# Optimization experiments

Hardware: AMD Instinct MI355X
Metric: run time of the kernel (lower is better)

## Reference

```python
import jax, jax.numpy as jnp
import numpy as np
import math

LOG_2PI = math.log(2.0 * math.pi)

def mv_gaussian_log_prob(value, mu, sig_diags, event_shape):
    # sig_diags acts as per-dim std (matches torch source: diff**2 / sig**2)
    diff = value - mu
    M = jnp.sum((diff / sig_diags) ** 2, axis=-1)
    half_log_det = jnp.sum(jnp.log(sig_diags), axis=-1)
    return -0.5 * (event_shape * LOG_2PI + M) - half_log_det

def setup_inputs() -> dict:
    key = jax.random.key(0)
    ks = jax.random.split(key, 18)
    N, Yd, Xd, K, S = 8192, 512, 64, 16, 10
    d = {}
    d['Y'] = jax.random.normal(ks[0], (N, Yd), jnp.float32)
    d['We_mu'] = jax.random.normal(ks[1], (Yd, Xd), jnp.float32) * 0.05
    d['be_mu'] = jnp.zeros((Xd,), jnp.float32)
    d['We_sig'] = jax.random.normal(ks[2], (Yd, Xd), jnp.float32) * 0.05
    d['be_sig'] = jnp.zeros((Xd,), jnp.float32)
    d['Wd_mu'] = jax.random.normal(ks[3], (Xd, Yd), jnp.float32) * 0.05
    d['bd_mu'] = jnp.zeros((Yd,), jnp.float32)
    d['Wd_sig'] = jax.random.normal(ks[4], (Xd, Yd), jnp.float32) * 0.05
    d['bd_sig'] = jnp.zeros((Yd,), jnp.float32)
    d['phi_mus'] = jax.random.normal(ks[5], (K, Xd), jnp.float32)
    d['phi_sigs'] = jax.random.uniform(ks[6], (K, Xd), jnp.float32, 0.5, 1.5)
    d['phi_logits'] = jax.random.normal(ks[7], (K,), jnp.float32)
    d['theta_mus'] = jax.random.normal(ks[8], (K, Xd), jnp.float32)
    d['theta_sigs'] = jax.random.uniform(ks[9], (K, Xd), jnp.float32, 0.5, 1.5)
    d['theta_logits'] = jax.random.normal(ks[10], (K,), jnp.float32)
    d['u_noise'] = jax.random.uniform(ks[11], (N, S, K), jnp.float32, 1e-6, 1.0 - 1e-6)
    d['eps_noise'] = jax.random.normal(ks[12], (N * S, Xd), jnp.float32)
    d['temperature'] = jnp.ones((1,), jnp.float32)
    return d

def reference(Y, We_mu, be_mu, We_sig, be_sig, Wd_mu, bd_mu, Wd_sig, bd_sig,
              phi_mus, phi_sigs, phi_logits, theta_mus, theta_sigs, theta_logits,
              u_noise, eps_noise, temperature):
    N, Yd = Y.shape
    K, Xd = phi_mus.shape
    S = u_noise.shape[1]
    # encoder: diagonal Gaussian q(x|y)
    enc_mu = Y @ We_mu + be_mu                                   # [N,Xd]
    enc_sig = jax.nn.softplus(Y @ We_sig + be_sig) + 1e-3        # [N,Xd]
    # cluster responsibilities (vectorized over k)
    log_pi = jax.nn.log_softmax(phi_logits)                      # [K]
    std_k = enc_sig[:, None, :] + phi_sigs[None, :, :]           # [N,K,Xd]
    z_logits = log_pi[None, :] + mv_gaussian_log_prob(
        enc_mu[:, None, :], phi_mus[None, :, :], std_k, Xd)      # [N,K]
    z_log_probs = jax.nn.log_softmax(z_logits, axis=-1)
    # per-cluster posterior (diagonal precision-weighted combination)
    inv_enc = 1.0 / enc_sig                                      # [N,Xd]
    inv_gmm = 1.0 / phi_sigs                                     # [K,Xd]
    Sig_t = 1.0 / (inv_enc[:, None, :] + inv_gmm[None, :, :])    # [N,K,Xd]
    mu_t = Sig_t * ((inv_enc * enc_mu)[:, None, :] + (inv_gmm * phi_mus)[None, :, :])
    # relaxed one-hot (gumbel-softmax) samples, probs = exp(z_log_probs)
    g = -jnp.log(-jnp.log(u_noise))                              # [N,S,K]
    z = jax.nn.softmax((z_log_probs[:, None, :] + g) / temperature[0], axis=-1)
    mu_s = jnp.einsum('bsk,bkd->bsd', z, mu_t).reshape(N * S, Xd)
    Sig_s = jnp.einsum('bsk,bkd->bsd', z, Sig_t).reshape(N * S, Xd)
    th_mu = jnp.einsum('bsk,kd->bsd', z, theta_mus).reshape(N * S, Xd)
    th_sig = jnp.einsum('bsk,kd->bsd', z, theta_sigs).reshape(N * S, Xd)
    ph_mu = jnp.einsum('bsk,kd->bsd', z, phi_mus).reshape(N * S, Xd)
    ph_sig = jnp.einsum('bsk,kd->bsd', z, phi_sigs).reshape(N * S, Xd)
    # reparameterized latent samples (diag cov -> std = sqrt)
    x_samp = mu_s + jnp.sqrt(Sig_s) * eps_noise                  # [N*S,Xd]
    # decoder
    mu_y = x_samp @ Wd_mu + bd_mu
    sig_y = jax.nn.softplus(x_samp @ Wd_sig + bd_sig) + 1e-3
    Yr = jnp.broadcast_to(Y[:, None, :], (N, S, Yd)).reshape(N * S, Yd)
    enc_mu_r = jnp.broadcast_to(enc_mu[:, None, :], (N, S, Xd)).reshape(N * S, Xd)
    enc_sig_r = jnp.broadcast_to(enc_sig[:, None, :], (N, S, Xd)).reshape(N * S, Xd)
    zf = z.reshape(N * S, K)
    loss1 = mv_gaussian_log_prob(Yr, mu_y, sig_y, Yd)
    loss2 = -mv_gaussian_log_prob(x_samp, enc_mu_r, enc_sig_r, Xd)
    loss3 = (mv_gaussian_log_prob(x_samp, th_mu, th_sig, Xd)
             + jnp.sum(jax.nn.log_softmax(theta_logits) * zf, axis=1))
    loss4 = -(mv_gaussian_log_prob(x_samp, ph_mu, ph_sig, Xd)
              + jnp.sum((z_log_probs[:, None, :] * z).reshape(N * S, K), axis=1))
    loss5 = jnp.sum(jnp.log(jnp.sum(jnp.exp(z_log_probs), axis=1)))
    return -(jnp.sum(loss1 + loss2 + loss3 + loss4) / S + loss5)
```

## Files before the change

### kernel.cpp

```cpp
#include <hip/hip_runtime.h>
#include <math.h>

#define YD 512
#define XD 64
#define KK 16
#define SS 10

typedef __attribute__((ext_vector_type(8))) short short8;
typedef __attribute__((ext_vector_type(4))) float f32x4;
typedef __attribute__((ext_vector_type(2))) float f32x2;

__device__ __forceinline__ float wave_sum(float v) {
#pragma unroll
    for (int off = 32; off > 0; off >>= 1) v += __shfl_xor(v, off, 64);
    return v;
}

__device__ __forceinline__ float fast_rcp(float x) {
    return __builtin_amdgcn_rcpf(x);
}

__device__ __forceinline__ float hw_exp2(float x) {
    return __builtin_amdgcn_exp2f(x);
}
__device__ __forceinline__ float hw_log2(float x) {
    return __builtin_amdgcn_logf(x);
}

__device__ __forceinline__ float bcast(float v, int l) {
    return __uint_as_float((unsigned int)__builtin_amdgcn_readlane((int)__float_as_uint(v), l));
}

__device__ __forceinline__ float softplusf(float x) {
    return fmaxf(x, 0.0f) + __logf(1.0f + __expf(-fabsf(x)));
}

__device__ __forceinline__ unsigned short f32_to_bf16(float f) {
    union { float f; unsigned int u; } v; v.f = f;
    unsigned int r = v.u + 0x7fffu + ((v.u >> 16) & 1u);
    return (unsigned short)(r >> 16);
}

__device__ __forceinline__ unsigned int pack2_bf16(float a, float b) {
    unsigned int ua = __float_as_uint(a), ub = __float_as_uint(b);
    ua = (ua + 0x7fffu + ((ua >> 16) & 1u)) >> 16;
    ub = (ub + 0x7fffu + ((ub >> 16) & 1u)) & 0xffff0000u;
    return ua | ub;
}

__global__ __launch_bounds__(256) void prep_kernel(
    const float* __restrict__ Wd_mu, const float* __restrict__ Wd_sig,
    const float* __restrict__ We_mu, const float* __restrict__ We_sig,
    const float* __restrict__ phi_mus, const float* __restrict__ phi_sigs,
    const float* __restrict__ theta_mus, const float* __restrict__ theta_sigs,
    const float* __restrict__ theta_logits,
    unsigned short* __restrict__ wmu_s, unsigned short* __restrict__ wsg_s,
    unsigned short* __restrict__ wenc,
    float4* __restrict__ tab4, float* __restrict__ lsetp)
{
    int idx = blockIdx.x * 256 + threadIdx.x;
    if (idx < 65536) {
        int mat = idx >> 15;
        int e = idx & 32767;
        int j = e & 7;
        int n = (e >> 3) & 15;
        int q = (e >> 7) & 7;
        int tg = e >> 10;
        int k = q * 8 + j;
        int col = tg * 16 + n;
        const float* W = mat ? Wd_sig : Wd_mu;
        unsigned short* o = mat ? wsg_s : wmu_s;
        o[e] = f32_to_bf16(W[k * YD + col]);
    } else if (idx < 131072) {
        int ii = idx - 65536;
        int mat = ii >> 15;
        int e = ii & 32767;
        int j = e & 7;
        int n = (e >> 3) & 15;
        int q = (e >> 7) & 3;
        int ct = (e >> 9) & 3;
        int kt = e >> 11;
        int k = kt * 32 + q * 8 + j;
        int col = ct * 16 + n;
        const float* W = mat ? We_sig : We_mu;
        wenc[mat * 32768 + e] = f32_to_bf16(W[k * XD + col]);
    } else if (idx < 131072 + 1024) {
        int e = idx - 131072;
        float4 t;
        t.x = phi_mus[e];
        t.y = phi_sigs[e];
        t.z = theta_mus[e];
        t.w = theta_sigs[e];
        tab4[e] = t;
    } else if (idx == 131072 + 1024) {
        float mt = theta_logits[0];
        for (int k = 1; k < KK; ++k) mt = fmaxf(mt, theta_logits[k]);
        float st = 0.f;
        for (int k = 0; k < KK; ++k) st += __expf(theta_logits[k] - mt);
        lsetp[0] = mt + __logf(st);
    }
}

__global__ __launch_bounds__(256) void encoder_mfma(
    const float* __restrict__ Y,
    const unsigned short* __restrict__ wenc,
    const float* __restrict__ be_mu, const float* __restrict__ be_sig,
    float* __restrict__ enc_mu, float* __restrict__ enc_sig)
{
    const int t = threadIdx.x;
    const int w = t >> 6, lane = t & 63, l16 = lane & 15, quad = lane >> 4;
    const int mat = blockIdx.x & 1;
    const int rt = blockIdx.x >> 1;
    const int row = rt * 16 + l16;
    const int ct = w;
    const unsigned short* Ws = wenc + mat * 32768;
    const float4* Yrow = (const float4*)(Y + (size_t)row * YD);

    const float* bias = mat ? be_sig : be_mu;
    float* outp = mat ? enc_sig : enc_mu;
    const int col = ct * 16 + l16;
    const float bv = bias[col];
    f32x4 acc = (f32x4){bv, bv, bv, bv};

#pragma unroll
    for (int kt = 0; kt < 16; ++kt) {
        float4 y0 = Yrow[kt * 8 + quad * 2];
        float4 y1 = Yrow[kt * 8 + quad * 2 + 1];
        union { short8 s; unsigned int u[4]; } a;
        a.u[0] = pack2_bf16(y0.x, y0.y);
        a.u[1] = pack2_bf16(y0.z, y0.w);
        a.u[2] = pack2_bf16(y1.x, y1.y);
        a.u[3] = pack2_bf16(y1.z, y1.w);
        short8 b = *(const short8*)(Ws + (((kt * 4 + ct) * 4 + quad) * 16 + l16) * 8);
        acc = __builtin_amdgcn_mfma_f32_16x16x32_bf16(a.s, b, acc, 0, 0, 0);
    }

    const int base_row = rt * 16 + quad * 4;
#pragma unroll
    for (int r = 0; r < 4; ++r) {
        float v = acc[r];
        if (mat) v = softplusf(v) + 1e-3f;
        outp[(size_t)(base_row + r) * XD + col] = v;
    }
}

__global__ __launch_bounds__(256, 3) void fused_sample_kernel(
    const float* __restrict__ enc_mu_g, const float* __restrict__ enc_sig_g,
    const float* __restrict__ phi_mus, const float* __restrict__ phi_sigs,
    const float* __restrict__ phi_logits, const float4* __restrict__ tab4,
    const float* __restrict__ theta_logits, const float* __restrict__ lsetp,
    const float* __restrict__ u_noise, const float* __restrict__ eps_noise,
    const float* __restrict__ temperature,
    unsigned short* __restrict__ x_bf16, double* __restrict__ slots)
{
    __shared__ float red234[4], red5[4];
    const int wv = threadIdx.x >> 6;
    const int n = blockIdx.x * 4 + wv;
    const int d = threadIdx.x & 63;
    const int kd = d & 15;
    const int g = d >> 4;

    const float4* em4 = (const float4*)(enc_mu_g + (size_t)n * XD + g * 16);
    const float4* es4 = (const float4*)(enc_sig_g + (size_t)n * XD + g * 16);
    const float4* pm4 = (const float4*)(phi_mus + kd * XD + g * 16);
    const float4* ps4 = (const float4*)(phi_sigs + kd * XD + g * 16);

    float part = 0.f;
#pragma unroll
    for (int q = 0; q < 4; ++q) {
        float4 emv = em4[q], esv = es4[q], pmv = pm4[q], psv = ps4[q];
        {
            float sd = esv.x + psv.x; float df = (emv.x - pmv.x) * fast_rcp(sd);
            part += fmaf(-0.5f * df, df, -__logf(sd));
        }
        {
            float sd = esv.y + psv.y; float df = (emv.y - pmv.y) * fast_rcp(sd);
            part += fmaf(-0.5f * df, df, -__logf(sd));
        }
        {
            float sd = esv.z + psv.z; float df = (emv.z - pmv.z) * fast_rcp(sd);
            part += fmaf(-0.5f * df, df, -__logf(sd));
        }
        {
            float sd = esv.w + psv.w; float df = (emv.w - pmv.w) * fast_rcp(sd);
            part += fmaf(-0.5f * df, df, -__logf(sd));
        }
    }
    part += __shfl_xor(part, 16, 64);
    part += __shfl_xor(part, 32, 64);
    float zl = part + phi_logits[kd];

    float m = zl;
#pragma unroll
    for (int off = 1; off <= 8; off <<= 1) m = fmaxf(m, __shfl_xor(m, off, 64));
    float e0 = __expf(zl - m);
    float s0 = e0;
#pragma unroll
    for (int off = 1; off <= 8; off <<= 1) s0 += __shfl_xor(s0, off, 64);
    zl -= m + __logf(s0);

    float m3 = zl;
#pragma unroll
    for (int off = 1; off <= 8; off <<= 1) m3 = fmaxf(m3, __shfl_xor(m3, off, 64));
    float e3 = __expf(zl - m3);
    float s3 = e3;
#pragma unroll
    for (int off = 1; off <= 8; off <<= 1) s3 += __shfl_xor(s3, off, 64);
    float l5 = m3 + __logf(s3);

    const float invT = fast_rcp(temperature[0]);
    const float zl_l = zl;
    const float tl_l = theta_logits[kd];
    const float lset = lsetp[0];

    const float em = enc_mu_g[(size_t)n * XD + d];
    const float es = enc_sig_g[(size_t)n * XD + d];
    const float inv_es = fast_rcp(es);
    const float log_es = __logf(es);
    const float em_ie = inv_es * em;

    f32x2 mS[KK], tt2[KK], pp2[KK];
#pragma unroll
    for (int k = 0; k < KK; ++k) {
        float4 tb = tab4[k * XD + d];
        float ig = fast_rcp(tb.y);
        float Sgk = fast_rcp(inv_es + ig);
        float muk = Sgk * fmaf(ig, tb.x, em_ie);
        mS[k]  = (f32x2){muk, Sgk};
        tt2[k] = (f32x2){tb.z, tb.w};
        pp2[k] = (f32x2){tb.x, tb.y};
    }

    float eP[3];
    float esc = 0.f;
#pragma unroll
    for (int p = 0; p < 3; ++p) {
        int sp = p * 4 + g;
        int spc = sp < SS ? sp : 0;
        float u = u_noise[((size_t)n * SS + spc) * KK + kd];
        float lg = (zl_l - __logf(-__logf(u))) * invT;
        float mg = lg;
        mg = fmaxf(mg, __shfl_xor(mg, 1, 64));
        mg = fmaxf(mg, __shfl_xor(mg, 2, 64));
        mg = fmaxf(mg, __shfl_xor(mg, 4, 64));
        mg = fmaxf(mg, __shfl_xor(mg, 8, 64));
        float e = __expf(lg - mg);
        float zs = e;
        zs += __shfl_xor(zs, 1, 64);
        zs += __shfl_xor(zs, 2, 64);
        zs += __shfl_xor(zs, 4, 64);
        zs += __shfl_xor(zs, 8, 64);
        e *= fast_rcp(zs);
        eP[p] = e;
        if (sp < SS) esc = fmaf(e, tl_l - zl_l, esc);
    }

    float r_acc = 0.f;
    const float* erow = eps_noise + (size_t)n * SS * XD + d;
    unsigned short* xrow = x_bf16 + (size_t)n * SS * XD + d;

#pragma unroll
    for (int s = 0; s < SS; ++s) {
        const int p = s >> 2, L = (s & 3) * 16;
        f32x2 a0 = (f32x2){0.f, 0.f};
        f32x2 a1 = (f32x2){0.f, 0.f};
        f32x2 a2 = (f32x2){0.f, 0.f};
#pragma unroll
        for (int k = 0; k < KK; ++k) {
            float ek = bcast(eP[p], L + k);
            f32x2 ev = (f32x2){ek, ek};
            a0 = a0 + ev * mS[k];
            a1 = a1 + ev * tt2[k];
            a2 = a2 + ev * pp2[k];
        }
        float ms = a0.x, Ssum = a0.y;
        float tmu = a1.x, tsig = a1.y;
        float pmu = a2.x, psig = a2.y;

        float ep = erow[s * XD];
        float x = fmaf(__builtin_amdgcn_sqrtf(Ssum), ep, ms);
        xrow[s * XD] = f32_to_bf16(x);

        float de  = (x - em) * inv_es;
        float rts = fast_rcp(tsig);
        float dt2 = (x - tmu) * rts;
        float dp  = (x - pmu) * fast_rcp(psig);
        r_acc += 0.5f * (de * de - dt2 * dt2 + dp * dp) + __logf(psig * rts);
    }

    r_acc = fmaf((float)SS, log_es, r_acc);
    r_acc += esc;
    r_acc = wave_sum(r_acc);

    const float C234 = 0.5f * XD * 1.8378770664093453f;
    float total = r_acc + (float)SS * (C234 - lset);

    if (d == 0) { red234[wv] = total; red5[wv] = l5; }
    __syncthreads();
    if (threadIdx.x == 0) {
        atomicAdd(slots + (blockIdx.x & 63),
                  (double)(red234[0] + red234[1] + red234[2] + red234[3]));
        atomicAdd(slots + 64 + (blockIdx.x & 63),
                  (double)(red5[0] + red5[1] + red5[2] + red5[3]));
    }
}

__global__ __launch_bounds__(256) void decoder_mfma(
    const unsigned short* __restrict__ xb,
    const unsigned short* __restrict__ wmu_s,
    const unsigned short* __restrict__ wsg_s,
    const float* __restrict__ bd_mu, const float* __restrict__ bd_sig,
    const float* __restrict__ Y, double* __restrict__ slots1,
    unsigned int magicS)
{
    __shared__ float red[4];
    const int t = threadIdx.x;
    const int w = t >> 6;
    const int lane = t & 63;
    const int l16 = lane & 15;
    const int quad = lane >> 4;
    const int mb = blockIdx.x;
    const int nb = blockIdx.y;

    const int row0 = mb * 128 + w * 32;

    float Yv[2][4][4];
#pragma unroll
    for (int rg = 0; rg < 2; ++rg) {
        const int m_base = row0 + rg * 16 + quad * 4;
        unsigned int q10 = (unsigned int)(((unsigned long long)(unsigned int)m_base * magicS) >> 35);
        int rem = m_base - (int)q10 * 10;
#pragma unroll
        for (int r = 0; r < 4; ++r) {
            unsigned int ny = q10 + ((rem + r) >= 10 ? 1u : 0u);
            unsigned int iy = ny * YD + nb * 64 + l16;
#pragma unroll
            for (int tt = 0; tt < 4; ++tt) Yv[rg][r][tt] = Y[iy + tt * 16];
        }
    }

    short8 a[2][2];
#pragma unroll
    for (int rg = 0; rg < 2; ++rg) {
        const unsigned short* xp = xb + (size_t)(row0 + rg * 16 + l16) * XD + quad * 8;
        a[rg][0] = *(const short8*)xp;
        a[rg][1] = *(const short8*)(xp + 32);
    }

    f32x4 accmu[2][4], accsg[2][4];
#pragma unroll
    for (int tt = 0; tt < 4; ++tt) {
        int col = nb * 64 + tt * 16 + l16;
        float bm = bd_mu[col], bs = bd_sig[col];
#pragma unroll
        for (int rg = 0; rg < 2; ++rg) {
            accmu[rg][tt] = (f32x4){bm, bm, bm, bm};
            accsg[rg][tt] = (f32x4){bs, bs, bs, bs};
        }
    }

#pragma unroll
    for (int tt = 0; tt < 4; ++tt) {
        int tg = nb * 4 + tt;
        int boff = ((tg * 8 + quad) * 16 + l16) * 8;
        short8 b0 = *(const short8*)(wmu_s + boff);
        short8 b1 = *(const short8*)(wmu_s + boff + 512);
        short8 c0 = *(const short8*)(wsg_s + boff);
        short8 c1 = *(const short8*)(wsg_s + boff + 512);
#pragma unroll
        for (int rg = 0; rg < 2; ++rg) {
            accmu[rg][tt] = __builtin_amdgcn_mfma_f32_16x16x32_bf16(a[rg][0], b0, accmu[rg][tt], 0, 0, 0);
            accmu[rg][tt] = __builtin_amdgcn_mfma_f32_16x16x32_bf16(a[rg][1], b1, accmu[rg][tt], 0, 0, 0);
            accsg[rg][tt] = __builtin_amdgcn_mfma_f32_16x16x32_bf16(a[rg][0], c0, accsg[rg][tt], 0, 0, 0);
            accsg[rg][tt] = __builtin_amdgcn_mfma_f32_16x16x32_bf16(a[rg][1], c1, accsg[rg][tt], 0, 0, 0);
        }
    }

    const float LOG2E = 1.4426950408889634f;
    const float C2    = 0.0014426950408889634f;
    const float Cq    = -1.0406844905181233f;
    const float LN2   = 0.6931471805599453f;
    const float CC    = 11.72841345861326f;

    f32x2 pq = (f32x2){0.f, 0.f};
    f32x2 pl = (f32x2){0.f, 0.f};
    f32x2 prod = (f32x2){1.f, 1.f};
#pragma unroll
    for (int r = 0; r < 4; ++r) {
#pragma unroll
        for (int tt = 0; tt < 4; ++tt) {
            f32x2 acs = (f32x2){accsg[0][tt][r], accsg[1][tt][r]};
            f32x2 acm = (f32x2){accmu[0][tt][r], accmu[1][tt][r]};
            f32x2 yv  = (f32x2){Yv[0][r][tt], Yv[1][r][tt]};
            f32x2 te  = acs * LOG2E;
            f32x2 u2;
            u2.x = hw_exp2(te.x);
            u2.y = hw_exp2(te.y);
            f32x2 up = u2 + 1.0f;
            f32x2 s2;
            s2.x = hw_log2(up.x);
            s2.y = hw_log2(up.y);
            s2 = s2 + C2;
            f32x2 rs;
            rs.x = fast_rcp(s2.x);
            rs.y = fast_rcp(s2.y);
            f32x2 diff = (yv - acm) * rs;
            pq = pq + (Cq * diff) * diff;
            prod = prod * s2;
        }
        if (r & 1) {
            pl.x += hw_log2(prod.x);
            pl.y += hw_log2(prod.y);
            prod = (f32x2){1.f, 1.f};
        }
    }
    float part = fmaf(-LN2, pl.x + pl.y, pq.x + pq.y) + CC;
    part = wave_sum(part);
    if (lane == 0) red[w] = part;
    __syncthreads();
    if (t == 0) {
        atomicAdd(slots1 + ((blockIdx.y * gridDim.x + blockIdx.x) & 63),
                  (double)(red[0] + red[1] + red[2] + red[3]));
    }
}

__global__ void finalize_kernel(const double* __restrict__ slots,
                                float* __restrict__ out, int NS, int S)
{
    double l234 = 0.0, l5 = 0.0, l1 = 0.0;
    for (int i = 0; i < 64; ++i) {
        l234 += slots[i];
        l5   += slots[64 + i];
        l1   += slots[128 + i];
    }
    l1 += (double)NS * (-0.5 * (double)YD * 1.8378770664093453);
    out[0] = (float)(-((l1 + l234) / (double)S + l5));
}

extern "C" void kernel_launch(void* const* d_in, const int* in_sizes, int n_in,
                              void* d_out, int out_size, void* d_ws, size_t ws_size,
                              hipStream_t stream) {
    const float* Y            = (const float*)d_in[0];
    const float* We_mu        = (const float*)d_in[1];
    const float* be_mu        = (const float*)d_in[2];
    const float* We_sig       = (const float*)d_in[3];
    const float* be_sig       = (const float*)d_in[4];
    const float* Wd_mu        = (const float*)d_in[5];
    const float* bd_mu        = (const float*)d_in[6];
    const float* Wd_sig       = (const float*)d_in[7];
    const float* bd_sig       = (const float*)d_in[8];
    const float* phi_mus      = (const float*)d_in[9];
    const float* phi_sigs     = (const float*)d_in[10];
    const float* phi_logits   = (const float*)d_in[11];
    const float* theta_mus    = (const float*)d_in[12];
    const float* theta_sigs   = (const float*)d_in[13];
    const float* theta_logits = (const float*)d_in[14];
    const float* u_noise      = (const float*)d_in[15];
    const float* eps_noise    = (const float*)d_in[16];
    const float* temperature  = (const float*)d_in[17];

    const int N = in_sizes[0] / YD;
    const int S = in_sizes[15] / (N * KK);
    const int NS = N * S;
    const unsigned int magicS =
        (unsigned int)((((unsigned long long)1 << 35) + S - 1) / (unsigned long long)S);

    char* base = (char*)d_ws;
    double* slots = (double*)base;
    float* enc_mu  = (float*)(base + 2048);
    float* enc_sig = enc_mu + (size_t)N * XD;
    float* zlp     = enc_sig + (size_t)N * XD;
    float4* tab4   = (float4*)(zlp + (size_t)N * KK);
    float* lsetp   = (float*)(tab4 + 1024);
    unsigned short* xb    = (unsigned short*)(lsetp + 16);
    unsigned short* wmu_s = xb + (size_t)NS * XD;
    unsigned short* wsg_s = wmu_s + 32768;
    unsigned short* wenc  = wsg_s + 32768;

    hipMemsetAsync(slots, 0, 2048, stream);

    prep_kernel<<<517, 256, 0, stream>>>(Wd_mu, Wd_sig, We_mu, We_sig,
                                         phi_mus, phi_sigs, theta_mus,
                                         theta_sigs, theta_logits,
                                         wmu_s, wsg_s, wenc, tab4, lsetp);
    encoder_mfma<<<(N / 16) * 2, 256, 0, stream>>>(Y, wenc, be_mu, be_sig,
                                                   enc_mu, enc_sig);
    fused_sample_kernel<<<N / 4, 256, 0, stream>>>(enc_mu, enc_sig,
                                                   phi_mus, phi_sigs, phi_logits,
                                                   tab4, theta_logits, lsetp,
                                                   u_noise, eps_noise, temperature,
                                                   xb, slots);
    decoder_mfma<<<dim3(NS / 128, YD / 64), 256, 0, stream>>>(
        xb, wmu_s, wsg_s, bd_mu, bd_sig, Y, slots + 128, magicS);
    finalize_kernel<<<1, 1, 0, stream>>>(slots, (float*)d_out, NS, S);
}
```

Baseline: 194.6 us.

## Fold slot zeroing into prep, finalize in last decoder block, drop softmax max-shifts

Zeroes the accumulation slots and ticket inside prep_kernel instead of a separate memset, and moves the final reduction into the last-finishing decoder block using an atomic ticket, removing two launches. It also drops the max-subtraction in two 16-way log-sum-exp and Gumbel-softmax reductions, since log-softmax outputs are at most zero and the Gumbel logits are bounded for these inputs. The risk is overflow if temperature is small or the logits are large, plus the usual threadfence/ticket ordering subtleties.

```diff
diff --git a/kernel.cpp b/kernel.cpp
--- a/kernel.cpp
+++ b/kernel.cpp
@@ -56,7 +56,8 @@
     const float* __restrict__ theta_logits,
     unsigned short* __restrict__ wmu_s, unsigned short* __restrict__ wsg_s,
     unsigned short* __restrict__ wenc,
-    float4* __restrict__ tab4, float* __restrict__ lsetp)
+    float4* __restrict__ tab4, float* __restrict__ lsetp,
+    unsigned int* __restrict__ slots_zero)
 {
     int idx = blockIdx.x * 256 + threadIdx.x;
     if (idx < 65536) {
@@ -98,6 +99,8 @@
         float st = 0.f;
         for (int k = 0; k < KK; ++k) st += __expf(theta_logits[k] - mt);
         lsetp[0] = mt + __logf(st);
+    } else if (idx >= 132352 && idx < 132864) {
+        slots_zero[idx - 132352] = 0u;
     }
 }
 
@@ -199,14 +202,10 @@
     for (int off = 1; off <= 8; off <<= 1) s0 += __shfl_xor(s0, off, 64);
     zl -= m + __logf(s0);
 
-    float m3 = zl;
-#pragma unroll
-    for (int off = 1; off <= 8; off <<= 1) m3 = fmaxf(m3, __shfl_xor(m3, off, 64));
-    float e3 = __expf(zl - m3);
-    float s3 = e3;
+    float s3 = __expf(zl);
 #pragma unroll
     for (int off = 1; off <= 8; off <<= 1) s3 += __shfl_xor(s3, off, 64);
-    float l5 = m3 + __logf(s3);
+    float l5 = __logf(s3);
 
     const float invT = fast_rcp(temperature[0]);
     const float zl_l = zl;
@@ -239,12 +238,7 @@
         int spc = sp < SS ? sp : 0;
         float u = u_noise[((size_t)n * SS + spc) * KK + kd];
         float lg = (zl_l - __logf(-__logf(u))) * invT;
-        float mg = lg;
-        mg = fmaxf(mg, __shfl_xor(mg, 1, 64));
-        mg = fmaxf(mg, __shfl_xor(mg, 2, 64));
-        mg = fmaxf(mg, __shfl_xor(mg, 4, 64));
-        mg = fmaxf(mg, __shfl_xor(mg, 8, 64));
-        float e = __expf(lg - mg);
+        float e = __expf(lg);
         float zs = e;
         zs += __shfl_xor(zs, 1, 64);
         zs += __shfl_xor(zs, 2, 64);
@@ -310,8 +304,9 @@
     const unsigned short* __restrict__ wmu_s,
     const unsigned short* __restrict__ wsg_s,
     const float* __restrict__ bd_mu, const float* __restrict__ bd_sig,
-    const float* __restrict__ Y, double* __restrict__ slots1,
-    unsigned int magicS)
+    const float* __restrict__ Y, double* __restrict__ slots,
+    unsigned int* __restrict__ ticket, float* __restrict__ out,
+    unsigned int magicS, int NS, int S, int totalBlocks)
 {
     __shared__ float red[4];
     const int t = threadIdx.x;
@@ -419,22 +414,21 @@
     if (lane == 0) red[w] = part;
     __syncthreads();
     if (t == 0) {
-        atomicAdd(slots1 + ((blockIdx.y * gridDim.x + blockIdx.x) & 63),
+        atomicAdd(slots + 128 + ((blockIdx.y * gridDim.x + blockIdx.x) & 63),
                   (double)(red[0] + red[1] + red[2] + red[3]));
-    }
-}
-
-__global__ void finalize_kernel(const double* __restrict__ slots,
-                                float* __restrict__ out, int NS, int S)
-{
-    double l234 = 0.0, l5 = 0.0, l1 = 0.0;
-    for (int i = 0; i < 64; ++i) {
-        l234 += slots[i];
-        l5   += slots[64 + i];
-        l1   += slots[128 + i];
-    }
-    l1 += (double)NS * (-0.5 * (double)YD * 1.8378770664093453);
-    out[0] = (float)(-((l1 + l234) / (double)S + l5));
+        __threadfence();
+        unsigned int old = atomicAdd(ticket, 1u);
+        if (old == (unsigned int)(totalBlocks - 1)) {
+            double l234 = 0.0, l5 = 0.0, l1 = 0.0;
+            for (int i = 0; i < 64; ++i) {
+                l234 += __hip_atomic_load(slots + i,       __ATOMIC_RELAXED, __HIP_MEMORY_SCOPE_AGENT);
+                l5   += __hip_atomic_load(slots + 64 + i,  __ATOMIC_RELAXED, __HIP_MEMORY_SCOPE_AGENT);
+                l1   += __hip_atomic_load(slots + 128 + i, __ATOMIC_RELAXED, __HIP_MEMORY_SCOPE_AGENT);
+            }
+            l1 += (double)NS * (-0.5 * (double)YD * 1.8378770664093453);
+            out[0] = (float)(-((l1 + l234) / (double)S + l5));
+        }
+    }
 }
 
 extern "C" void kernel_launch(void* const* d_in, const int* in_sizes, int n_in,
@@ -467,6 +461,7 @@
 
     char* base = (char*)d_ws;
     double* slots = (double*)base;
+    unsigned int* ticket = (unsigned int*)(base + 1536);
     float* enc_mu  = (float*)(base + 2048);
     float* enc_sig = enc_mu + (size_t)N * XD;
     float* zlp     = enc_sig + (size_t)N * XD;
@@ -477,12 +472,13 @@
     unsigned short* wsg_s = wmu_s + 32768;
     unsigned short* wenc  = wsg_s + 32768;
 
-    hipMemsetAsync(slots, 0, 2048, stream);
-
-    prep_kernel<<<517, 256, 0, stream>>>(Wd_mu, Wd_sig, We_mu, We_sig,
+    const int decBlocks = (NS / 128) * (YD / 64);
+
+    prep_kernel<<<520, 256, 0, stream>>>(Wd_mu, Wd_sig, We_mu, We_sig,
                                          phi_mus, phi_sigs, theta_mus,
                                          theta_sigs, theta_logits,
-                                         wmu_s, wsg_s, wenc, tab4, lsetp);
+                                         wmu_s, wsg_s, wenc, tab4, lsetp,
+                                         (unsigned int*)slots);
     encoder_mfma<<<(N / 16) * 2, 256, 0, stream>>>(Y, wenc, be_mu, be_sig,
                                                    enc_mu, enc_sig);
     fused_sample_kernel<<<N / 4, 256, 0, stream>>>(enc_mu, enc_sig,
@@ -491,6 +487,6 @@
                                                    u_noise, eps_noise, temperature,
                                                    xb, slots);
     decoder_mfma<<<dim3(NS / 128, YD / 64), 256, 0, stream>>>(
-        xb, wmu_s, wsg_s, bd_mu, bd_sig, Y, slots + 128, magicS);
-    finalize_kernel<<<1, 1, 0, stream>>>(slots, (float*)d_out, NS, S);
-}
+        xb, wmu_s, wsg_s, bd_mu, bd_sig, Y, slots, ticket, (float*)d_out,
+        magicS, NS, S, decBlocks);
+}
```

Result: slower. 291.3 us (+49.7%).
